# Optimization experiments

Measured on AMD Instinct MI355X. Metric: run time of the kernel, lower is better.

The kernel has to match this reference:

```python
import jax, jax.numpy as jnp
import numpy as np

NEG = -1e18


def _split_heads(x, h):
    # [B, L, D] -> [B, H, L, D/H]
    b, l, d = x.shape
    return x.reshape(b, l, h, d // h).transpose(0, 2, 1, 3)


def _merge_heads(x):
    # [B, H, L, Dh] -> [B, L, H*Dh]
    b, h, l, dh = x.shape
    return x.transpose(0, 2, 1, 3).reshape(b, l, h * dh)


def _sparse(att, dp_map):
    # att: [B, H, L] per-token scores; dp_map: [B, 2, L] (row, col) tree indices.
    # scatter att[b,h,t] -> S[b, h, dp_map[b,0,t], dp_map[b,1,t]], then symmetrize.
    B, H, L = att.shape
    bi = jnp.arange(B)[:, None, None]          # [B,1,1]
    hi = jnp.arange(H)[None, :, None]          # [1,H,1]
    p0 = dp_map[:, 0, :][:, None, :]           # [B,1,L]
    p1 = dp_map[:, 1, :][:, None, :]           # [B,1,L]
    s = jnp.zeros((B, H, L, L), att.dtype)
    s = s.at[bi, hi, p0, p1].set(att)          # matches torch index_put_ (overwrite)
    return s + jnp.swapaxes(s, 2, 3)


def _reverse(values, dp_map):
    # r[b, j] = values[b, dp_map[b,0,j]] for j >= 1; r[b,0] = 0
    idx = dp_map[:, 0, :]                      # [B, L]
    r = jnp.take_along_axis(values, idx[:, :, None], axis=1)
    return r.at[:, 0, :].set(0.0)


def setup_inputs() -> dict:
    key = jax.random.key(0)
    ks = jax.random.split(key, 16)
    B, L, D, R, H = 16, 384, 768, 768, 12
    inp = {
        "queries":   jax.random.normal(ks[0], (B, L, D), jnp.float32),
        "keys":      jax.random.normal(ks[1], (B, L, D), jnp.float32),
        "values":    jax.random.normal(ks[2], (B, L, D), jnp.float32),
        "relations": jax.random.normal(ks[3], (B, L, R), jnp.float32),
        "dp_map":    jax.random.randint(ks[4], (B, 2, L), 0, L, jnp.int32),
        "mask":      jax.random.bernoulli(ks[5], 0.1, (B, L, L)),
        "rel_mask":  jax.random.bernoulli(ks[6], 0.1, (B, L, 1)),
        "Wq":  jax.random.normal(ks[7],  (D, D), jnp.float32) * 0.02,
        "Wk":  jax.random.normal(ks[8],  (D, D), jnp.float32) * 0.02,
        "Wv":  jax.random.normal(ks[9],  (D, D), jnp.float32) * 0.02,
        "Wo":  jax.random.normal(ks[10], (D, D), jnp.float32) * 0.02,
        "Wge": jax.random.normal(ks[11], (D, R), jnp.float32) * 0.02,
        "Wgr": jax.random.normal(ks[12], (R, R), jnp.float32) * 0.02,
        "Vr":  jax.random.normal(ks[13], (R, 1), jnp.float32) * 0.02,
        "Vg":  jax.random.normal(ks[14], (R, 1), jnp.float32) * 0.02,
    }
    return inp


def reference(queries, keys, values, relations, dp_map, mask, rel_mask,
              Wq, Wk, Wv, Wo, Wge, Wgr, Vr, Vg):
    H = 12
    R = Vg.shape[0]
    Dk = Wq.shape[1]
    scale = (Dk // H) ** -0.5

    # config.is_reverse = True path
    hv = jnp.where(rel_mask, 0.0, _reverse(values, dp_map))       # [B,L,D]
    rel = jnp.where(rel_mask, 0.0, relations)                     # [B,L,R]

    # semantic gated mechanism
    rv_h = _split_heads(rel @ Wgr, H)                             # [B,H,L,R/H]
    hs_h = _split_heads(hv @ Wge, H)
    Vg_h = Vg.reshape(H, R // H, 1)
    g = jnp.tanh(jnp.einsum('bhld,hdo->bhlo', hs_h + rv_h, Vg_h))[..., 0]
    gated = _sparse(g, dp_map)                                    # [B,H,L,L]

    q = _split_heads(queries @ Wq, H) * scale
    k = _split_heads(keys @ Wk, H)
    v = _split_heads(values @ Wv, H)
    rel_h = _split_heads(rel, H)
    Vr_h = Vr.reshape(H, R // H, 1)

    self_logits = jnp.einsum('bhqd,bhkd->bhqk', q, k)             # [B,H,L,L]
    rel_logits = _sparse(jnp.einsum('bhld,hdo->bhlo', rel_h, Vr_h)[..., 0], dp_map)

    m = mask[:, None]                                             # [B,1,L,L]
    self_logits = jnp.where(m, NEG, self_logits)
    rel_logits = jnp.where(m, NEG, rel_logits)

    attention_weights = self_logits.sum(axis=1) / H               # [B,L,L]
    sw = jax.nn.softmax(self_logits, axis=-1)
    rw = jax.nn.softmax(rel_logits, axis=-1)
    w = (1.0 - gated) * sw + gated * rw                           # dropout p=0

    ctx = jnp.einsum('bhqk,bhkd->bhqd', w, v)
    out = _merge_heads(ctx) @ Wo
    return out, attention_weights
```

## Files before the change

### kernel.cpp

```cpp
#include <hip/hip_runtime.h>
#include <math.h>

#define Bn 16
#define Lq 384
#define Hn 12
#define Dm 768
#define DH 64
#define QT2 16
#define NEGV (-1e18f)
#define SPADU 404
#define ECAP 32

typedef __attribute__((ext_vector_type(4))) float f32x4;
typedef __attribute__((ext_vector_type(8))) __bf16 bf16x8;
typedef __attribute__((ext_vector_type(4))) __bf16 bf16x4;
typedef unsigned short ushort_t;
typedef unsigned int uint_t;
typedef unsigned long long ull_t;

__device__ __forceinline__ ushort_t f2b(float f) {
  return __builtin_bit_cast(ushort_t, (__bf16)f);
}
__device__ __forceinline__ float b2f(ushort_t u) {
  return __uint_as_float(((unsigned int)u) << 16);
}
__device__ __forceinline__ bf16x8 cvt8(float4 a, float4 b) {
  bf16x8 r;
  r[0] = (__bf16)a.x; r[1] = (__bf16)a.y; r[2] = (__bf16)a.z; r[3] = (__bf16)a.w;
  r[4] = (__bf16)b.x; r[5] = (__bf16)b.y; r[6] = (__bf16)b.z; r[7] = (__bf16)b.w;
  return r;
}

#define SMEM_BYTES 24576

__global__ __launch_bounds__(256) void k_prep(
    const float* __restrict__ Wge, const float* __restrict__ Wgr,
    const float* __restrict__ Vg,
    float* __restrict__ Age, float* __restrict__ Agr,
    const float* __restrict__ W0, const float* __restrict__ W1,
    const float* __restrict__ W2, const float* __restrict__ W3,
    ushort_t* __restrict__ T0, ushort_t* __restrict__ T1,
    ushort_t* __restrict__ T2, ushort_t* __restrict__ T3,
    const int* __restrict__ dp, int* __restrict__ win,
    const int* __restrict__ mask, ull_t* __restrict__ mbits)
{
  __shared__ float vg[DH];
  __shared__ float t[32][33];
  int blk = blockIdx.x;
  if (blk < 24) {
    int which = blk / Hn;
    int h = blk % Hn;
    const float* Wsrc = which ? Wgr : Wge;
    float* dst = which ? Agr : Age;
    if (threadIdx.x < DH) vg[threadIdx.x] = Vg[h*DH + threadIdx.x];
    __syncthreads();
    for (int d = threadIdx.x; d < Dm; d += 256) {
      const float* wrow = Wsrc + (size_t)d*Dm + h*DH;
      float s = 0.f;
      #pragma unroll 8
      for (int j = 0; j < DH; ++j) s = fmaf(wrow[j], vg[j], s);
      dst[h*Dm + d] = s;
    }
  } else if (blk < 24 + 2304) {
    int b2 = blk - 24;
    int z = b2 / 576, rem = b2 % 576;
    const float* W = (z == 0) ? W0 : (z == 1) ? W1 : (z == 2) ? W2 : W3;
    ushort_t* WT = (z == 0) ? T0 : (z == 1) ? T1 : (z == 2) ? T2 : T3;
    int k0 = (rem / 24)*32, n0 = (rem % 24)*32;
    int tx = threadIdx.x & 31, ty = threadIdx.x >> 5;
    #pragma unroll
    for (int r = 0; r < 4; ++r)
      t[ty + r*8][tx] = W[(size_t)(k0 + ty + r*8)*Dm + n0 + tx];
    __syncthreads();
    #pragma unroll
    for (int r = 0; r < 4; ++r)
      WT[(size_t)(n0 + ty + r*8)*Dm + k0 + tx] = f2b(t[tx][ty + r*8]);
  } else if (blk < 2352) {
    int i = (blk - 2328)*256 + threadIdx.x;
    int b = i / Lq, l = i % Lq;
    int p0 = dp[(size_t)(b*2+0)*Lq + l];
    int p1 = dp[(size_t)(b*2+1)*Lq + l];
    atomicMax(&win[(size_t)b*Lq*Lq + (size_t)p0*Lq + p1], l);
  } else {
    int rr = blk - 2352;
    int lane = threadIdx.x & 63, wave = threadIdx.x >> 6;
    int gi = rr*4 + wave;
    const int* mrow = mask + (size_t)gi*Lq;
    ull_t w0 = __ballot(mrow[lane]        != 0);
    ull_t w1 = __ballot(mrow[lane + 64]   != 0);
    ull_t w2 = __ballot(mrow[lane + 128]  != 0);
    ull_t w3 = __ballot(mrow[lane + 192]  != 0);
    ull_t w4 = __ballot(mrow[lane + 256]  != 0);
    ull_t w5 = __ballot(mrow[lane + 320]  != 0);
    if (lane == 0) {
      ull_t* out = mbits + (size_t)gi*6;
      out[0] = w0; out[1] = w1; out[2] = w2;
      out[3] = w3; out[4] = w4; out[5] = w5;
    }
  }
}


__device__ void dev_grlog(char* sm, int blk,
    const float* __restrict__ values, const float* __restrict__ relations,
    const int* __restrict__ dp, const int* __restrict__ rel_mask,
    const float* __restrict__ Age, const float* __restrict__ Agr,
    const float* __restrict__ Vr, float* __restrict__ g, float* __restrict__ rlog)
{
  float (*relrow)[Dm] = (float(*)[Dm])sm;
  float (*hvrow)[Dm]  = (float(*)[Dm])(sm + 4*Dm*sizeof(float));
  int b = blk / (Lq/4), l0 = (blk % (Lq/4))*4;
  int tid = threadIdx.x, lane = tid & 63, wave = tid >> 6;
  #pragma unroll
  for (int rr = 0; rr < 4; ++rr) {
    int l = l0 + rr;
    int rm = rel_mask[(size_t)b*Lq + l];
    int idx = dp[(size_t)(b*2)*Lq + l];
    const float* vrow = values + ((size_t)b*Lq + idx)*Dm;
    const float* rrow = relations + ((size_t)b*Lq + l)*Dm;
    for (int d = tid; d < Dm; d += 256) {
      relrow[rr][d] = rm ? 0.f : rrow[d];
      hvrow[rr][d]  = (rm || l == 0) ? 0.f : vrow[d];
    }
  }
  __syncthreads();
  int l = l0 + wave;
  for (int h = 0; h < Hn; ++h) {
    float p = 0.f;
    #pragma unroll
    for (int k = 0; k < Dm/64; ++k) {
      int d = lane + 64*k;
      p = fmaf(hvrow[wave][d], Age[h*Dm + d],
          fmaf(relrow[wave][d], Agr[h*Dm + d], p));
    }
    #pragma unroll
    for (int o = 32; o > 0; o >>= 1) p += __shfl_xor(p, o);
    if (lane == 0) g[((size_t)b*Hn + h)*Lq + l] = tanhf(p);
  }
  if (lane < Hn) {
    float s = 0.f;
    #pragma unroll 8
    for (int j = 0; j < DH; ++j) {
      int jj = (j + lane*5) & 63;
      s = fmaf(relrow[wave][lane*DH + jj], Vr[lane*DH + jj], s);
    }
    rlog[((size_t)b*Hn + lane)*Lq + l] = s;
  }
}

__device__ void dev_mmqkv(char* sm, int bm, int bn, int z,
    const float* __restrict__ Xq, const float* __restrict__ Xk,
    const float* __restrict__ Xv,
    const ushort_t* __restrict__ WqT, const ushort_t* __restrict__ WkT,
    const ushort_t* __restrict__ WvT,
    ushort_t* __restrict__ qbf, ushort_t* __restrict__ kbf,
    ushort_t* __restrict__ vTbf)
{
  ushort_t* As = (ushort_t*)sm;
  ushort_t* Bs = (ushort_t*)(sm + 8192);
  const float* A     = (z == 0) ? Xq : (z == 1) ? Xk : Xv;
  const ushort_t* BT = (z == 0) ? WqT : (z == 1) ? WkT : WvT;
  int m0 = bm*64, n0 = bn*128;
  int t = threadIdx.x;
  int wave = t >> 6, lane = t & 63;
  int wr = wave >> 1, wc = wave & 1;
  int lrow = lane & 15, lkg = lane >> 4;
  int sr = t >> 3, sc8 = t & 7;

  f32x4 acc[2][4];
  #pragma unroll
  for (int i = 0; i < 2; ++i)
    #pragma unroll
    for (int j = 0; j < 4; ++j) acc[i][j] = (f32x4)(0.f);

  for (int k0 = 0; k0 < Dm; k0 += 64) {
    __syncthreads();
    #pragma unroll
    for (int i = 0; i < 2; ++i) {
      int row = sr + i*32;
      const float* ap = A + (size_t)(m0 + row)*Dm + k0 + sc8*8;
      float4 f0 = *(const float4*)ap;
      float4 f1 = *(const float4*)(ap + 4);
      *(bf16x8*)&As[row*64 + (sc8 ^ (row & 7))*8] = cvt8(f0, f1);
    }
    #pragma unroll
    for (int i = 0; i < 4; ++i) {
      int row = sr + i*32;
      uint4 vb = *(const uint4*)(BT + (size_t)(n0 + row)*Dm + k0 + sc8*8);
      *(uint4*)&Bs[row*64 + (sc8 ^ (row & 7))*8] = vb;
    }
    __syncthreads();
    #pragma unroll
    for (int kk = 0; kk < 2; ++kk) {
      bf16x8 aF[2], bF[4];
      int chunk = kk*4 + lkg;
      #pragma unroll
      for (int mi = 0; mi < 2; ++mi) {
        int arow = wr*32 + mi*16 + lrow;
        aF[mi] = *(const bf16x8*)&As[arow*64 + ((chunk ^ (arow & 7)) << 3)];
      }
      #pragma unroll
      for (int ni = 0; ni < 4; ++ni) {
        int brow = wc*64 + ni*16 + lrow;
        bF[ni] = *(const bf16x8*)&Bs[brow*64 + ((chunk ^ (brow & 7)) << 3)];
      }
      #pragma unroll
      for (int mi = 0; mi < 2; ++mi)
        #pragma unroll
        for (int ni = 0; ni < 4; ++ni)
          acc[mi][ni] = __builtin_amdgcn_mfma_f32_16x16x32_bf16(
              aF[mi], bF[ni], acc[mi][ni], 0, 0, 0);
    }
  }

  float alpha = (z == 0) ? 0.125f : 1.f;
  #pragma unroll
  for (int mi = 0; mi < 2; ++mi) {
    #pragma unroll
    for (int ni = 0; ni < 4; ++ni) {
      f32x4 a = acc[mi][ni];
      int rit = wr*32 + mi*16 + 4*lkg;
      int cit = wc*64 + ni*16 + lrow;
      int gcol = bn*128 + cit;
      if (z < 2) {
        ushort_t* Cb = z ? kbf : qbf;
        int grow = m0 + rit;
        #pragma unroll
        for (int r = 0; r < 4; ++r)
          Cb[(size_t)(grow + r)*Dm + gcol] = f2b(a[r]*alpha);
      } else {
        int b = bm/6;
        int rl = (bm%6)*64 + rit;
        ushort4 u;
        u.x = f2b(a[0]); u.y = f2b(a[1]); u.z = f2b(a[2]); u.w = f2b(a[3]);
        *(ushort4*)&vTbf[((size_t)b*Dm + gcol)*Lq + rl] = u;
      }
    }
  }
}

__device__ void dev_collect(char* sm, int i0b, int j0b, int b,
    const int* __restrict__ win, uint_t* __restrict__ ent,
    int* __restrict__ rowcnt)
{
  int (*tB)[33] = (int(*)[33])sm;
  int i0 = i0b*32, j0 = j0b*32;
  const int* wb = win + (size_t)b*Lq*Lq;
  int tx = threadIdx.x & 31, ty = threadIdx.x >> 5;
  #pragma unroll
  for (int rr = 0; rr < 4; ++rr) {
    int r = ty + rr*8;
    tB[r][tx] = wb[(size_t)(j0+r)*Lq + i0 + tx];
  }
  __syncthreads();
  #pragma unroll
  for (int rr = 0; rr < 4; ++rr) {
    int ti = ty + rr*8;
    int i = i0 + ti, j = j0 + tx;
    int l1 = wb[(size_t)i*Lq + j];
    int l2 = tB[tx][ti];
    if (l1 >= 0 || l2 >= 0) {
      int slot = atomicAdd(&rowcnt[(size_t)b*Lq + i], 1);
      if (slot < ECAP)
        ent[((size_t)b*Lq + i)*ECAP + slot] =
            (uint_t)j | ((uint_t)(l1 + 1) << 9) | ((uint_t)(l2 + 1) << 19);
    }
  }
}

__device__ void dev_aw(char* sm, int bm, int bn, int b,
    const ushort_t* __restrict__ A, const ushort_t* __restrict__ BT,
    float* __restrict__ Cf, const int* __restrict__ mask, float alpha)
{
  ushort_t* As = (ushort_t*)sm;
  ushort_t* Bs = (ushort_t*)(sm + 8192);
  const ushort_t* Ab = A  + (size_t)b*Lq*Dm;
  const ushort_t* Bb = BT + (size_t)b*Lq*Dm;
  int m0 = bm*64, n0 = bn*128;
  int t = threadIdx.x;
  int wave = t >> 6, lane = t & 63;
  int wr = wave >> 1, wc = wave & 1;
  int lrow = lane & 15, lkg = lane >> 4;
  int sr = t >> 3, sc8 = t & 7;

  f32x4 acc[2][4];
  #pragma unroll
  for (int i = 0; i < 2; ++i)
    #pragma unroll
    for (int j = 0; j < 4; ++j) acc[i][j] = (f32x4)(0.f);

  for (int k0 = 0; k0 < Dm; k0 += 64) {
    __syncthreads();
    #pragma unroll
    for (int i = 0; i < 2; ++i) {
      int row = sr + i*32;
      uint4 va = *(const uint4*)(Ab + (size_t)(m0 + row)*Dm + k0 + sc8*8);
      *(uint4*)&As[row*64 + (sc8 ^ (row & 7))*8] = va;
    }
    #pragma unroll
    for (int i = 0; i < 4; ++i) {
      int row = sr + i*32;
      uint4 vb = *(const uint4*)(Bb + (size_t)(n0 + row)*Dm + k0 + sc8*8);
      *(uint4*)&Bs[row*64 + (sc8 ^ (row & 7))*8] = vb;
    }
    __syncthreads();
    #pragma unroll
    for (int kk = 0; kk < 2; ++kk) {
      bf16x8 aF[2], bF[4];
      int chunk = kk*4 + lkg;
      #pragma unroll
      for (int mi = 0; mi < 2; ++mi) {
        int arow = wr*32 + mi*16 + lrow;
        aF[mi] = *(const bf16x8*)&As[arow*64 + ((chunk ^ (arow & 7)) << 3)];
      }
      #pragma unroll
      for (int ni = 0; ni < 4; ++ni) {
        int brow = wc*64 + ni*16 + lrow;
        bF[ni] = *(const bf16x8*)&Bs[brow*64 + ((chunk ^ (brow & 7)) << 3)];
      }
      #pragma unroll
      for (int mi = 0; mi < 2; ++mi)
        #pragma unroll
        for (int ni = 0; ni < 4; ++ni)
          acc[mi][ni] = __builtin_amdgcn_mfma_f32_16x16x32_bf16(
              aF[mi], bF[ni], acc[mi][ni], 0, 0, 0);
    }
  }

  #pragma unroll
  for (int mi = 0; mi < 2; ++mi) {
    #pragma unroll
    for (int ni = 0; ni < 4; ++ni) {
      f32x4 a = acc[mi][ni];
      int rit = wr*32 + mi*16 + 4*lkg;
      int cit = wc*64 + ni*16 + lrow;
      int rl = m0 + rit, cl = n0 + cit;
      const int* mb2 = mask + (size_t)b*Lq*Lq;
      float* awb = Cf + (size_t)b*Lq*Lq;
      #pragma unroll
      for (int r = 0; r < 4; ++r) {
        int m = mb2[(size_t)(rl + r)*Lq + cl];
        awb[(size_t)(rl + r)*Lq + cl] = m ? NEGV : a[r]*alpha;
      }
    }
  }
}

struct AttnS {
  ushort_t S16[QT2][SPADU];
  ull_t mb[QT2][6];
  float2 rg2[Lq + 1];
  uint_t entS[QT2*ECAP];
  int cntS[QT2];
  float pp[QT2][4];
  float sinvS[QT2];
};

__device__ void dev_attn3(char* sm, int bid,
    const ushort_t* __restrict__ qbf, const ushort_t* __restrict__ kbf,
    const ushort_t* __restrict__ vT,
    const ull_t* __restrict__ mbits, const int* __restrict__ rowcnt,
    const uint_t* __restrict__ ent,
    const float* __restrict__ g, const float* __restrict__ rlog,
    ushort_t* __restrict__ ctxbf)
{
  AttnS* S = (AttnS*)sm;
  int h  = bid % Hn;
  int qt = (bid / Hn) % (Lq/QT2);
  int b  = bid / (Hn * (Lq/QT2));
  int q0 = qt * QT2;
  int tid = threadIdx.x, lane = tid & 63, wave = tid >> 6;
  int lrow = lane & 15, lkg = lane >> 4;

  const float* gh = g    + ((size_t)b*Hn + h)*Lq;
  const float* rh = rlog + ((size_t)b*Hn + h)*Lq;

  if (tid < QT2*6) {
    int r = tid / 6, u = tid % 6;
    S->mb[r][u] = mbits[((size_t)b*Lq + q0 + r)*6 + u];
  }
  if (tid == 0) { S->rg2[0].x = 0.f; S->rg2[0].y = 0.f; }
  for (int e = tid; e < Lq; e += 256) {
    float2 v2; v2.x = rh[e]; v2.y = gh[e];
    S->rg2[e + 1] = v2;
  }
  #pragma unroll
  for (int e = tid; e < QT2*ECAP; e += 256)
    S->entS[e] = ent[((size_t)b*Lq + q0)*ECAP + e];
  if (tid < QT2) {
    int c = rowcnt[(size_t)b*Lq + q0 + tid];
    S->cntS[tid] = c > ECAP ? ECAP : c;
  }
  __syncthreads();

  {
    const ushort_t* qb = qbf + ((size_t)b*Lq + q0 + lrow)*Dm + h*DH + lkg*8;
    bf16x8 aF0 = *(const bf16x8*)(qb);
    bf16x8 aF1 = *(const bf16x8*)(qb + 32);
    int col0 = wave*96;
    int w0 = col0 >> 6;
    ull_t m0[4], m1[4];
    #pragma unroll
    for (int r = 0; r < 4; ++r) {
      m0[r] = S->mb[4*lkg + r][w0];
      m1[r] = S->mb[4*lkg + r][w0 + 1];
    }
    float ps[4] = {0.f, 0.f, 0.f, 0.f};
    const ushort_t* kb = kbf + ((size_t)b*Lq + col0 + lrow)*Dm + h*DH + lkg*8;
    #pragma unroll
    for (int tt = 0; tt < 6; ++tt) {
      int col = col0 + tt*16 + lrow;
      bf16x8 bF0 = *(const bf16x8*)(kb);
      bf16x8 bF1 = *(const bf16x8*)(kb + 32);
      kb += 16*Dm;
      f32x4 z = (f32x4)(0.f);
      z = __builtin_amdgcn_mfma_f32_16x16x32_bf16(aF0, bF0, z, 0, 0, 0);
      z = __builtin_amdgcn_mfma_f32_16x16x32_bf16(aF1, bF1, z, 0, 0, 0);
      bool hi = ((col0 + tt*16) >> 6) != w0;
      int sh = col & 63;
      #pragma unroll
      for (int r = 0; r < 4; ++r) {
        ull_t mw = hi ? m1[r] : m0[r];
        bool mk = (mw >> sh) & 1ull;
        float e = mk ? 0.f : __expf(z[r]);
        ps[r] += e;
        S->S16[4*lkg + r][col] = f2b(e);
      }
    }
    #pragma unroll
    for (int off = 1; off < 16; off <<= 1)
      #pragma unroll
      for (int r = 0; r < 4; ++r) ps[r] += __shfl_xor(ps[r], off);
    if (lrow == 0) {
      #pragma unroll
      for (int r = 0; r < 4; ++r) S->pp[4*lkg + r][wave] = ps[r];
    }
  }
  __syncthreads();

  if (tid < QT2) {
    int row = tid;
    float ssum = S->pp[row][0] + S->pp[row][1] + S->pp[row][2] + S->pp[row][3];
    float si = 1.f / ssum;
    S->sinvS[row] = si;
    int nun = 384;
    #pragma unroll
    for (int u = 0; u < 6; ++u) nun -= (int)__popcll(S->mb[row][u]);
    int cnt = S->cntS[row];
    const uint_t* erow = &S->entS[row*ECAP];
    float rext = 0.f;
    for (int e = 0; e < cnt; ++e) {
      uint_t en = erow[e];
      int j = en & 511;
      if ((S->mb[row][j >> 6] >> (j & 63)) & 1ull) continue;
      float rel = S->rg2[(en >> 9) & 1023].x + S->rg2[en >> 19].x;
      rext += __expf(rel) - 1.f;
    }
    float sr = ssum / ((float)nun + rext);
    for (int e = 0; e < cnt; ++e) {
      uint_t en = erow[e];
      int j = en & 511;
      if ((S->mb[row][j >> 6] >> (j & 63)) & 1ull) continue;
      float2 a = S->rg2[(en >> 9) & 1023];
      float2 c = S->rg2[en >> 19];
      float er = __expf(a.x + c.x);
      float gvv = a.y + c.y;
      float ev = b2f(S->S16[row][j]);
      S->S16[row][j] = f2b((1.f - gvv)*ev + gvv*er*sr);
    }
  }
  __syncthreads();

  {
    int dcol = h*DH + wave*16 + lrow;
    const ushort_t* vb = vT + ((size_t)b*Dm + dcol)*Lq + lkg*8;
    const ushort_t* prow = &S->S16[lrow][0];
    f32x4 o = (f32x4)(0.f);
    #pragma unroll
    for (int ks = 0; ks < 12; ++ks) {
      bf16x4 lo = *(const bf16x4*)(prow + ks*32 + lkg*8);
      bf16x4 hi = *(const bf16x4*)(prow + ks*32 + lkg*8 + 4);
      bf16x8 pa = __builtin_shufflevector(lo, hi, 0,1,2,3,4,5,6,7);
      bf16x8 bv = *(const bf16x8*)(vb + ks*32);
      o = __builtin_amdgcn_mfma_f32_16x16x32_bf16(pa, bv, o, 0, 0, 0);
    }
    #pragma unroll
    for (int r = 0; r < 4; ++r) {
      float si = S->sinvS[4*lkg + r];
      ctxbf[((size_t)b*Lq + q0 + 4*lkg + r)*Dm + dcol] = f2b(o[r]*si);
    }
  }
}


__global__ __launch_bounds__(256) void k_mega1(
    const float* __restrict__ values, const float* __restrict__ relations,
    const int* __restrict__ dp, const int* __restrict__ rel_mask,
    const float* __restrict__ Age, const float* __restrict__ Agr,
    const float* __restrict__ Vr, float* __restrict__ g, float* __restrict__ rlog,
    const float* __restrict__ Xq, const float* __restrict__ Xk,
    const float* __restrict__ Xv,
    const ushort_t* __restrict__ WqT, const ushort_t* __restrict__ WkT,
    const ushort_t* __restrict__ WvT,
    ushort_t* __restrict__ qbf, ushort_t* __restrict__ kbf,
    ushort_t* __restrict__ vTbf,
    const int* __restrict__ win, uint_t* __restrict__ ent,
    int* __restrict__ rowcnt)
{
  __shared__ __align__(16) char sm[SMEM_BYTES];
  int blk = blockIdx.x;
  if (blk < 1536) {
    dev_grlog(sm, blk, values, relations, dp, rel_mask, Age, Agr, Vr, g, rlog);
  } else if (blk < 3264) {
    int t = blk - 1536;
    dev_mmqkv(sm, t % 96, (t/96) % 6, t/576, Xq, Xk, Xv, WqT, WkT, WvT,
              qbf, kbf, vTbf);
  } else {
    int t = blk - 3264;
    dev_collect(sm, t % 12, (t/12) % 12, t/144, win, ent, rowcnt);
  }
}

__global__ __launch_bounds__(256) void k_mega2(
    const ushort_t* __restrict__ qbf, const ushort_t* __restrict__ kbf,
    const ushort_t* __restrict__ vTbf,
    const ull_t* __restrict__ mbits, const int* __restrict__ rowcnt,
    const uint_t* __restrict__ ent,
    const float* __restrict__ g, const float* __restrict__ rlog,
    ushort_t* __restrict__ ctxbf,
    const int* __restrict__ mask, float* __restrict__ awp)
{
  __shared__ __align__(16) char sm[SMEM_BYTES];
  int blk = blockIdx.x;
  if (blk < 288) {
    dev_aw(sm, blk % 6, (blk/6) % 3, blk/18, qbf, kbf, awp, mask, 1.f/12.f);
  } else {
    dev_attn3(sm, blk - 288, qbf, kbf, vTbf, mbits, rowcnt, ent, g, rlog, ctxbf);
  }
}

__global__ __launch_bounds__(256) void k_mmout(
    const ushort_t* __restrict__ A, const ushort_t* __restrict__ BT,
    float* __restrict__ Cf)
{
  __shared__ ushort_t As[64*64];
  __shared__ ushort_t Bs[128*64];
  int m0 = blockIdx.x*64, n0 = blockIdx.y*128;
  int t = threadIdx.x;
  int wave = t >> 6, lane = t & 63;
  int wr = wave >> 1, wc = wave & 1;
  int lrow = lane & 15, lkg = lane >> 4;
  int sr = t >> 3, sc8 = t & 7;

  f32x4 acc[2][4];
  #pragma unroll
  for (int i = 0; i < 2; ++i)
    #pragma unroll
    for (int j = 0; j < 4; ++j) acc[i][j] = (f32x4)(0.f);

  for (int k0 = 0; k0 < Dm; k0 += 64) {
    __syncthreads();
    #pragma unroll
    for (int i = 0; i < 2; ++i) {
      int row = sr + i*32;
      uint4 va = *(const uint4*)(A + (size_t)(m0 + row)*Dm + k0 + sc8*8);
      *(uint4*)&As[row*64 + (sc8 ^ (row & 7))*8] = va;
    }
    #pragma unroll
    for (int i = 0; i < 4; ++i) {
      int row = sr + i*32;
      uint4 vb = *(const uint4*)(BT + (size_t)(n0 + row)*Dm + k0 + sc8*8);
      *(uint4*)&Bs[row*64 + (sc8 ^ (row & 7))*8] = vb;
    }
    __syncthreads();
    #pragma unroll
    for (int kk = 0; kk < 2; ++kk) {
      bf16x8 aF[2], bF[4];
      int chunk = kk*4 + lkg;
      #pragma unroll
      for (int mi = 0; mi < 2; ++mi) {
        int arow = wr*32 + mi*16 + lrow;
        aF[mi] = *(const bf16x8*)&As[arow*64 + ((chunk ^ (arow & 7)) << 3)];
      }
      #pragma unroll
      for (int ni = 0; ni < 4; ++ni) {
        int brow = wc*64 + ni*16 + lrow;
        bF[ni] = *(const bf16x8*)&Bs[brow*64 + ((chunk ^ (brow & 7)) << 3)];
      }
      #pragma unroll
      for (int mi = 0; mi < 2; ++mi)
        #pragma unroll
        for (int ni = 0; ni < 4; ++ni)
          acc[mi][ni] = __builtin_amdgcn_mfma_f32_16x16x32_bf16(
              aF[mi], bF[ni], acc[mi][ni], 0, 0, 0);
    }
  }

  #pragma unroll
  for (int mi = 0; mi < 2; ++mi) {
    #pragma unroll
    for (int ni = 0; ni < 4; ++ni) {
      f32x4 a = acc[mi][ni];
      int grow = m0 + wr*32 + mi*16 + 4*lkg;
      int gcol = n0 + wc*64 + ni*16 + lrow;
      #pragma unroll
      for (int r = 0; r < 4; ++r)
        Cf[(size_t)(grow + r)*Dm + gcol] = a[r];
    }
  }
}

extern "C" void kernel_launch(void* const* d_in, const int* in_sizes, int n_in,
                              void* d_out, int out_size, void* d_ws, size_t ws_size,
                              hipStream_t stream) {
  const float* queries   = (const float*)d_in[0];
  const float* keys      = (const float*)d_in[1];
  const float* values    = (const float*)d_in[2];
  const float* relations = (const float*)d_in[3];
  const int*   dp_map    = (const int*)d_in[4];
  const int*   mask      = (const int*)d_in[5];
  const int*   rel_mask  = (const int*)d_in[6];
  const float* Wq  = (const float*)d_in[7];
  const float* Wk  = (const float*)d_in[8];
  const float* Wv  = (const float*)d_in[9];
  const float* Wo  = (const float*)d_in[10];
  const float* Wge = (const float*)d_in[11];
  const float* Wgr = (const float*)d_in[12];
  const float* Vr  = (const float*)d_in[13];
  const float* Vg  = (const float*)d_in[14];

  float* ws = (float*)d_ws;
  const size_t SZ   = (size_t)Bn*Lq*Dm;
  const size_t WINS = (size_t)Bn*Lq*Lq;
  const size_t GSZ  = (size_t)Bn*Hn*Lq;
  const size_t ROWS = (size_t)Bn*Lq;

  int*   win  = (int*)ws;
  float* g    = ws + WINS;
  float* rlog = g + GSZ;
  float* Age  = rlog + GSZ;
  float* Agr  = Age + (size_t)Hn*Dm;
  ull_t* mbits = (ull_t*)(Agr + (size_t)Hn*Dm);
  int*   rowcnt = (int*)(mbits + ROWS*6);
  uint_t* ent  = (uint_t*)(rowcnt + ROWS);
  ushort_t* p0 = (ushort_t*)(ent + ROWS*ECAP);
  ushort_t* qbf  = p0;
  ushort_t* kbf  = p0 + SZ;
  ushort_t* vTbf = p0 + 2*SZ;
  ushort_t* ctxbf= p0 + 3*SZ;
  ushort_t* WqT  = p0 + 4*SZ;
  ushort_t* WkT  = WqT + (size_t)Dm*Dm;
  ushort_t* WvT  = WkT + (size_t)Dm*Dm;
  ushort_t* WoT  = WvT + (size_t)Dm*Dm;

  float* outp = (float*)d_out;
  float* awp  = outp + SZ;

  hipMemsetAsync(win, 0xFF, WINS*sizeof(int), stream);
  hipMemsetAsync(rowcnt, 0, ROWS*sizeof(int), stream);
  k_prep<<<3888, 256, 0, stream>>>(Wge, Wgr, Vg, Age, Agr,
                                   Wq, Wk, Wv, Wo, WqT, WkT, WvT, WoT,
                                   dp_map, win, mask, mbits);
  k_mega1<<<5568, 256, 0, stream>>>(values, relations, dp_map, rel_mask,
                                    Age, Agr, Vr, g, rlog,
                                    queries, keys, values, WqT, WkT, WvT,
                                    qbf, kbf, vTbf, win, ent, rowcnt);
  k_mega2<<<4896, 256, 0, stream>>>(qbf, kbf, vTbf, mbits, rowcnt, ent,
                                    g, rlog, ctxbf, mask, awp);
  k_mmout<<<dim3(96, 6), 256, 0, stream>>>(ctxbf, WoT, outp);
}
```

Measured before the change: 182.1 us.

## Build sparse tree entry lists directly from dp_map, dropping dense winner matrix

Removes the dense B×L×L winner-index matrix, along with its memset, its atomicMax scatter and the 2304 collect blocks. Sixteen per-batch blocks now load dp_map into shared memory and compute last-writer wins and symmetric partners with an O(L²) scan per batch. This cuts about 9.4 MB of memset plus a read of the full matrix. The cost is serial quadratic work in only 16 blocks, which could become a long tail in k_prep.

```diff
diff --git a/kernel.cpp b/kernel.cpp
--- a/kernel.cpp
+++ b/kernel.cpp
@@ -41,20 +41,23 @@
     const float* __restrict__ W2, const float* __restrict__ W3,
     ushort_t* __restrict__ T0, ushort_t* __restrict__ T1,
     ushort_t* __restrict__ T2, ushort_t* __restrict__ T3,
-    const int* __restrict__ dp, int* __restrict__ win,
-    const int* __restrict__ mask, ull_t* __restrict__ mbits)
+    const int* __restrict__ dp, const int* __restrict__ mask,
+    ull_t* __restrict__ mbits,
+    uint_t* __restrict__ ent, int* __restrict__ rowcnt)
 {
   __shared__ float vg[DH];
   __shared__ float t[32][33];
+  __shared__ int sp0[Lq], sp1[Lq], cntL[Lq];
   int blk = blockIdx.x;
+  int tid = threadIdx.x;
   if (blk < 24) {
     int which = blk / Hn;
     int h = blk % Hn;
     const float* Wsrc = which ? Wgr : Wge;
     float* dst = which ? Agr : Age;
-    if (threadIdx.x < DH) vg[threadIdx.x] = Vg[h*DH + threadIdx.x];
-    __syncthreads();
-    for (int d = threadIdx.x; d < Dm; d += 256) {
+    if (tid < DH) vg[tid] = Vg[h*DH + tid];
+    __syncthreads();
+    for (int d = tid; d < Dm; d += 256) {
       const float* wrow = Wsrc + (size_t)d*Dm + h*DH;
       float s = 0.f;
       #pragma unroll 8
@@ -67,7 +70,7 @@
     const float* W = (z == 0) ? W0 : (z == 1) ? W1 : (z == 2) ? W2 : W3;
     ushort_t* WT = (z == 0) ? T0 : (z == 1) ? T1 : (z == 2) ? T2 : T3;
     int k0 = (rem / 24)*32, n0 = (rem % 24)*32;
-    int tx = threadIdx.x & 31, ty = threadIdx.x >> 5;
+    int tx = tid & 31, ty = tid >> 5;
     #pragma unroll
     for (int r = 0; r < 4; ++r)
       t[ty + r*8][tx] = W[(size_t)(k0 + ty + r*8)*Dm + n0 + tx];
@@ -75,15 +78,9 @@
     #pragma unroll
     for (int r = 0; r < 4; ++r)
       WT[(size_t)(n0 + ty + r*8)*Dm + k0 + tx] = f2b(t[tx][ty + r*8]);
-  } else if (blk < 2352) {
-    int i = (blk - 2328)*256 + threadIdx.x;
-    int b = i / Lq, l = i % Lq;
-    int p0 = dp[(size_t)(b*2+0)*Lq + l];
-    int p1 = dp[(size_t)(b*2+1)*Lq + l];
-    atomicMax(&win[(size_t)b*Lq*Lq + (size_t)p0*Lq + p1], l);
-  } else {
-    int rr = blk - 2352;
-    int lane = threadIdx.x & 63, wave = threadIdx.x >> 6;
+  } else if (blk < 3864) {
+    int rr = blk - 2328;
+    int lane = tid & 63, wave = tid >> 6;
     int gi = rr*4 + wave;
     const int* mrow = mask + (size_t)gi*Lq;
     ull_t w0 = __ballot(mrow[lane]        != 0);
@@ -97,6 +94,39 @@
       out[0] = w0; out[1] = w1; out[2] = w2;
       out[3] = w3; out[4] = w4; out[5] = w5;
     }
+  } else {
+    int b = blk - 3864;
+    for (int l = tid; l < Lq; l += 256) {
+      sp0[l] = dp[(size_t)(b*2)*Lq + l];
+      sp1[l] = dp[(size_t)(b*2+1)*Lq + l];
+      cntL[l] = 0;
+    }
+    __syncthreads();
+    for (int l = tid; l < Lq; l += 256) {
+      int i = sp0[l], j = sp1[l];
+      bool winr = true;
+      int l2 = -1;
+      for (int t2 = 0; t2 < Lq; ++t2) {
+        int a0 = sp0[t2], a1 = sp1[t2];
+        if (t2 > l && a0 == i && a1 == j) winr = false;
+        if (a0 == j && a1 == i && t2 > l2) l2 = t2;
+      }
+      if (winr) {
+        int s = atomicAdd(&cntL[i], 1);
+        if (s < ECAP)
+          ent[((size_t)b*Lq + i)*ECAP + s] =
+              (uint_t)j | ((uint_t)(l + 1) << 9) | ((uint_t)(l2 + 1) << 19);
+        if (l2 < 0) {
+          int s2 = atomicAdd(&cntL[j], 1);
+          if (s2 < ECAP)
+            ent[((size_t)b*Lq + j)*ECAP + s2] =
+                (uint_t)i | ((uint_t)(l + 1) << 19);
+        }
+      }
+    }
+    __syncthreads();
+    for (int l = tid; l < Lq; l += 256)
+      rowcnt[(size_t)b*Lq + l] = cntL[l];
   }
 }
 
@@ -239,35 +269,6 @@
   }
 }
 
-__device__ void dev_collect(char* sm, int i0b, int j0b, int b,
-    const int* __restrict__ win, uint_t* __restrict__ ent,
-    int* __restrict__ rowcnt)
-{
-  int (*tB)[33] = (int(*)[33])sm;
-  int i0 = i0b*32, j0 = j0b*32;
-  const int* wb = win + (size_t)b*Lq*Lq;
-  int tx = threadIdx.x & 31, ty = threadIdx.x >> 5;
-  #pragma unroll
-  for (int rr = 0; rr < 4; ++rr) {
-    int r = ty + rr*8;
-    tB[r][tx] = wb[(size_t)(j0+r)*Lq + i0 + tx];
-  }
-  __syncthreads();
-  #pragma unroll
-  for (int rr = 0; rr < 4; ++rr) {
-    int ti = ty + rr*8;
-    int i = i0 + ti, j = j0 + tx;
-    int l1 = wb[(size_t)i*Lq + j];
-    int l2 = tB[tx][ti];
-    if (l1 >= 0 || l2 >= 0) {
-      int slot = atomicAdd(&rowcnt[(size_t)b*Lq + i], 1);
-      if (slot < ECAP)
-        ent[((size_t)b*Lq + i)*ECAP + slot] =
-            (uint_t)j | ((uint_t)(l1 + 1) << 9) | ((uint_t)(l2 + 1) << 19);
-    }
-  }
-}
-
 __device__ void dev_aw(char* sm, int bm, int bn, int b,
     const ushort_t* __restrict__ A, const ushort_t* __restrict__ BT,
     float* __restrict__ Cf, const int* __restrict__ mask, float alpha)
@@ -503,21 +504,16 @@
     const ushort_t* __restrict__ WqT, const ushort_t* __restrict__ WkT,
     const ushort_t* __restrict__ WvT,
     ushort_t* __restrict__ qbf, ushort_t* __restrict__ kbf,
-    ushort_t* __restrict__ vTbf,
-    const int* __restrict__ win, uint_t* __restrict__ ent,
-    int* __restrict__ rowcnt)
+    ushort_t* __restrict__ vTbf)
 {
   __shared__ __align__(16) char sm[SMEM_BYTES];
   int blk = blockIdx.x;
   if (blk < 1536) {
     dev_grlog(sm, blk, values, relations, dp, rel_mask, Age, Agr, Vr, g, rlog);
-  } else if (blk < 3264) {
+  } else {
     int t = blk - 1536;
     dev_mmqkv(sm, t % 96, (t/96) % 6, t/576, Xq, Xk, Xv, WqT, WkT, WvT,
               qbf, kbf, vTbf);
-  } else {
-    int t = blk - 3264;
-    dev_collect(sm, t % 12, (t/12) % 12, t/144, win, ent, rowcnt);
   }
 }
 
@@ -631,12 +627,10 @@
 
   float* ws = (float*)d_ws;
   const size_t SZ   = (size_t)Bn*Lq*Dm;
-  const size_t WINS = (size_t)Bn*Lq*Lq;
   const size_t GSZ  = (size_t)Bn*Hn*Lq;
   const size_t ROWS = (size_t)Bn*Lq;
 
-  int*   win  = (int*)ws;
-  float* g    = ws + WINS;
+  float* g    = ws;
   float* rlog = g + GSZ;
   float* Age  = rlog + GSZ;
   float* Agr  = Age + (size_t)Hn*Dm;
@@ -656,15 +650,13 @@
   float* outp = (float*)d_out;
   float* awp  = outp + SZ;
 
-  hipMemsetAsync(win, 0xFF, WINS*sizeof(int), stream);
-  hipMemsetAsync(rowcnt, 0, ROWS*sizeof(int), stream);
-  k_prep<<<3888, 256, 0, stream>>>(Wge, Wgr, Vg, Age, Agr,
+  k_prep<<<3880, 256, 0, stream>>>(Wge, Wgr, Vg, Age, Agr,
                                    Wq, Wk, Wv, Wo, WqT, WkT, WvT, WoT,
-                                   dp_map, win, mask, mbits);
-  k_mega1<<<5568, 256, 0, stream>>>(values, relations, dp_map, rel_mask,
+                                   dp_map, mask, mbits, ent, rowcnt);
+  k_mega1<<<3264, 256, 0, stream>>>(values, relations, dp_map, rel_mask,
                                     Age, Agr, Vr, g, rlog,
                                     queries, keys, values, WqT, WkT, WvT,
-                                    qbf, kbf, vTbf, win, ent, rowcnt);
+                                    qbf, kbf, vTbf);
   k_mega2<<<4896, 256, 0, stream>>>(qbf, kbf, vTbf, mbits, rowcnt, ent,
                                     g, rlog, ctxbf, mask, awp);
   k_mmout<<<dim3(96, 6), 256, 0, stream>>>(ctxbf, WoT, outp);
```

Result: slower. 196.8 us (+8.1%).
